# Kernel tuning notes

Measured on AMD Instinct MI355X. Metric: run time of the kernel, lower is better.

Reference implementation:

```python
import jax, jax.numpy as jnp
import numpy as np

B, L, D, H = 4, 1024, 1024, 16
HS = D // H
BLOCK = 1024
EPS = 1e-5


def setup_inputs() -> dict:
    key = jax.random.key(0)
    ks = jax.random.split(key, 12)
    s = 0.02
    return {
        "x": jax.random.normal(ks[0], (B, L, D), jnp.float32),
        "ln1_w": jnp.ones((D,), jnp.float32),
        "ln1_b": jnp.zeros((D,), jnp.float32),
        "Wqkv": jax.random.normal(ks[1], (D, 3 * D), jnp.float32) * s,
        "bqkv": jnp.zeros((3 * D,), jnp.float32),
        "Wproj": jax.random.normal(ks[2], (D, D), jnp.float32) * s,
        "bproj": jnp.zeros((D,), jnp.float32),
        "Er": jax.random.normal(ks[3], (BLOCK, HS), jnp.float32) * s,
        "ln2_w": jnp.ones((D,), jnp.float32),
        "ln2_b": jnp.zeros((D,), jnp.float32),
        "Wfc": jax.random.normal(ks[4], (D, 4 * D), jnp.float32) * s,
        "bfc": jnp.zeros((4 * D,), jnp.float32),
        "Wfc2": jax.random.normal(ks[5], (4 * D, D), jnp.float32) * s,
        "bfc2": jnp.zeros((D,), jnp.float32),
    }


def _layernorm(x, w, b):
    mu = jnp.mean(x, axis=-1, keepdims=True)
    var = jnp.mean(jnp.square(x - mu), axis=-1, keepdims=True)
    return (x - mu) * jax.lax.rsqrt(var + EPS) * w + b


def _skew(QEr):
    # Music-Transformer skew: pad one zero column on the left of last dim,
    # reshape (B,H,L,L+1) -> (B,H,L+1,L), drop first row.
    b, h, l, _ = QEr.shape
    padded = jnp.pad(QEr, ((0, 0), (0, 0), (0, 0), (1, 0)))
    return padded.reshape(b, h, l + 1, l)[:, :, 1:, :]


def _block(x, ln1_w, ln1_b, Wqkv, bqkv, Wproj, bproj, Er,
           ln2_w, ln2_b, Wfc, bfc, Wfc2, bfc2):
    b, l, d = x.shape
    # --- attention on ln_1(x) ---
    h = _layernorm(x, ln1_w, ln1_b)
    qkv = h @ Wqkv + bqkv                      # (B, L, 3D)
    q, k, v = jnp.split(qkv, 3, axis=-1)
    q = q.reshape(b, l, H, HS).transpose(0, 2, 1, 3)  # (B,H,L,hs)
    k = k.reshape(b, l, H, HS).transpose(0, 2, 1, 3)
    v = v.reshape(b, l, H, HS).transpose(0, 2, 1, 3)

    start = BLOCK - l
    Er_t = Er[start:, :].T                     # (hs, L)
    QEr = jnp.einsum('bhld,dm->bhlm', q, Er_t)  # (B,H,L,L)
    Srel = _skew(QEr)

    QKt = jnp.einsum('bhld,bhmd->bhlm', q, k)  # (B,H,L,L)
    scale = 1.0 / jnp.sqrt(jnp.asarray(HS, x.dtype))
    att = (QKt + Srel) * scale
    causal = jnp.tril(jnp.ones((l, l), bool))
    att = jnp.where(causal, att, jnp.asarray(-jnp.inf, att.dtype))
    att = jax.nn.softmax(att, axis=-1)
    y = jnp.einsum('bhlm,bhmd->bhld', att, v)  # (B,H,L,hs)
    y = y.transpose(0, 2, 1, 3).reshape(b, l, d)
    a = y @ Wproj + bproj

    x = x + a
    # --- MLP on ln_2(x) ---
    h2 = _layernorm(x, ln2_w, ln2_b)
    m = jax.nn.gelu(h2 @ Wfc + bfc, approximate=False) @ Wfc2 + bfc2
    return x + m


def reference(x, ln1_w, ln1_b, Wqkv, bqkv, Wproj, bproj, Er,
              ln2_w, ln2_b, Wfc, bfc, Wfc2, bfc2):
    return _block(x, ln1_w, ln1_b, Wqkv, bqkv, Wproj, bproj, Er,
                  ln2_w, ln2_b, Wfc, bfc, Wfc2, bfc2)
```

## Files before the change

### kernel.cpp

```cpp
#include <hip/hip_runtime.h>
#include <hip/hip_bf16.h>
#include <math.h>

typedef __attribute__((ext_vector_type(8))) __bf16 bf16x8;
typedef __attribute__((ext_vector_type(4))) float f32x4;

#define LL 1024
#define DD 1024
#define HH 16

#define GLOAD16(g, l)                                              \
  __builtin_amdgcn_global_load_lds(                                \
      (const __attribute__((address_space(1))) void*)(g),          \
      (__attribute__((address_space(3))) void*)(l), 16, 0, 0)

#define FENCE asm volatile("" ::: "memory")
#define BARRIER do { FENCE; __builtin_amdgcn_s_barrier(); FENCE; } while (0)
#define SCHEDB __builtin_amdgcn_sched_barrier(0)

__global__ __launch_bounds__(256) void transpose_cvt(const float* __restrict__ W,
                                                     __hip_bfloat16* __restrict__ Wt,
                                                     int R, int C) {
  __shared__ float tile[32][33];
  int tx = threadIdx.x;
  int r0 = blockIdx.y * 32, c0 = blockIdx.x * 32;
  int r = tx >> 3, c4 = (tx & 7) * 4;
  float4 v = *(const float4*)&W[(size_t)(r0 + r) * C + c0 + c4];
  tile[r][c4 + 0] = v.x; tile[r][c4 + 1] = v.y;
  tile[r][c4 + 2] = v.z; tile[r][c4 + 3] = v.w;
  __syncthreads();
  int c = tx >> 3, r4 = (tx & 7) * 4;
  __hip_bfloat16 o[4];
#pragma unroll
  for (int j = 0; j < 4; ++j) o[j] = __float2bfloat16(tile[r4 + j][c]);
  *(uint2*)&Wt[(size_t)(c0 + c) * R + r0 + r4] = *(const uint2*)o;
}

__global__ __launch_bounds__(256) void cvt_er(const float* __restrict__ Er,
                                              __hip_bfloat16* __restrict__ Erb) {
  int i = blockIdx.x * 256 + threadIdx.x;
  float4 v = *(const float4*)&Er[(size_t)i * 4];
  __hip_bfloat16 o[4];
  o[0] = __float2bfloat16(v.x); o[1] = __float2bfloat16(v.y);
  o[2] = __float2bfloat16(v.z); o[3] = __float2bfloat16(v.w);
  *(uint2*)&Erb[(size_t)i * 4] = *(const uint2*)o;
}

__global__ __launch_bounds__(256) void ln_kernel(const float* __restrict__ X,
                                                 const float* __restrict__ w,
                                                 const float* __restrict__ b,
                                                 __hip_bfloat16* __restrict__ out) {
  int row = blockIdx.x;
  int tid = threadIdx.x;
  const float* xr = X + (size_t)row * DD;
  float4 v = *(const float4*)&xr[tid * 4];
  float s = v.x + v.y + v.z + v.w;
  float s2 = v.x * v.x + v.y * v.y + v.z * v.z + v.w * v.w;
#pragma unroll
  for (int m = 1; m < 64; m <<= 1) {
    s += __shfl_xor(s, m);
    s2 += __shfl_xor(s2, m);
  }
  __shared__ float ps[4], ps2[4];
  int wv_ = tid >> 6, lane = tid & 63;
  if (lane == 0) { ps[wv_] = s; ps2[wv_] = s2; }
  __syncthreads();
  float ts = ps[0] + ps[1] + ps[2] + ps[3];
  float ts2 = ps2[0] + ps2[1] + ps2[2] + ps2[3];
  float mu = ts * (1.0f / DD);
  float var = ts2 * (1.0f / DD) - mu * mu;
  float rs = rsqrtf(var + 1e-5f);
  float4 wv = *(const float4*)&w[tid * 4];
  float4 bv = *(const float4*)&b[tid * 4];
  __hip_bfloat16 o[4];
  o[0] = __float2bfloat16((v.x - mu) * rs * wv.x + bv.x);
  o[1] = __float2bfloat16((v.y - mu) * rs * wv.y + bv.y);
  o[2] = __float2bfloat16((v.z - mu) * rs * wv.z + bv.z);
  o[3] = __float2bfloat16((v.w - mu) * rs * wv.w + bv.w);
  *(uint2*)&out[(size_t)row * DD + tid * 4] = *(const uint2*)o;
}

template <int EPI>
__global__ __launch_bounds__(512) void gemm256(const __hip_bfloat16* __restrict__ A,
                                               const __hip_bfloat16* __restrict__ Bt,
                                               const float* __restrict__ bias,
                                               const float* __restrict__ resid,
                                               void* __restrict__ Cout,
                                               int M, int N, int K) {
  __shared__ __hip_bfloat16 Ab[2][2][128][64];
  __shared__ __hip_bfloat16 Bb[2][2][128][64];
  const int tid = threadIdx.x, lane = tid & 63, w = tid >> 6;
  const int wm = w >> 2, wn = w & 3;

  int nbx = gridDim.x, nwg = nbx * gridDim.y;
  int orig = blockIdx.y * nbx + blockIdx.x;
  int cpx = nwg >> 3;
  int wgid = (orig & 7) * cpx + (orig >> 3);
  int bm0 = (wgid / nbx) * 256, bn0 = (wgid % nbx) * 256;

  const int srow = lane >> 3;
  const int scol = ((lane & 7) ^ srow) * 8;
  const int fr = lane & 15, kq = lane >> 4;

  auto stageA = [&](int d, int half, int k0) {
    const __hip_bfloat16* g0 =
        A + (size_t)(bm0 + half * 128 + w * 16 + srow) * K + k0 + scol;
    char* dst = (char*)&Ab[d][half][0][0] + w * 2048;
    GLOAD16(g0, dst);
    GLOAD16(g0 + (size_t)8 * K, dst + 1024);
  };
  auto stageB = [&](int d, int half, int k0) {
    const __hip_bfloat16* g0 =
        Bt + (size_t)(bn0 + half * 128 + w * 16 + srow) * K + k0 + scol;
    char* dst = (char*)&Bb[d][half][0][0] + w * 2048;
    GLOAD16(g0, dst);
    GLOAD16(g0 + (size_t)8 * K, dst + 1024);
  };
  auto ldA = [&](int d, int r, int ks) -> bf16x8 {
    int byte = r * 128 + (((ks * 32 + kq * 8) * 2) ^ ((r & 7) << 4));
    return *(const bf16x8*)((const char*)&Ab[d][wm][0][0] + byte);
  };
  auto ldB = [&](int d, int r, int ks) -> bf16x8 {
    int byte = r * 128 + (((ks * 32 + kq * 8) * 2) ^ ((r & 7) << 4));
    return *(const bf16x8*)((const char*)&Bb[d][wn >> 1][0][0] + byte);
  };

  f32x4 acc[8][4] = {};
  bf16x8 a0[8], a1[8], b0[4], b1[4];

  auto rdA = [&](bf16x8* dst, int d, int mfb) {
#pragma unroll
    for (int mf = 0; mf < 4; ++mf)
#pragma unroll
      for (int ks = 0; ks < 2; ++ks)
        dst[mf * 2 + ks] = ldA(d, (mfb + mf) * 16 + fr, ks);
  };
  auto rdB = [&](bf16x8* dst, int d, int nfb) {
#pragma unroll
    for (int nf = 0; nf < 2; ++nf)
#pragma unroll
      for (int ks = 0; ks < 2; ++ks)
        dst[nf * 2 + ks] = ldB(d, (wn & 1) * 64 + (nfb + nf) * 16 + fr, ks);
  };
  auto mmq = [&](int mo, int no, bf16x8* ar, bf16x8* br) {
    __builtin_amdgcn_s_setprio(1);
#pragma unroll
    for (int mf = 0; mf < 4; ++mf)
#pragma unroll
      for (int nf = 0; nf < 2; ++nf)
#pragma unroll
        for (int ks = 0; ks < 2; ++ks)
          acc[mo + mf][no + nf] = __builtin_amdgcn_mfma_f32_16x16x32_bf16(
              ar[mf * 2 + ks], br[nf * 2 + ks], acc[mo + mf][no + nf], 0, 0, 0);
    __builtin_amdgcn_s_setprio(0);
  };

  stageA(0, 0, 0); stageA(0, 1, 0);
  stageB(0, 0, 0); stageB(0, 1, 0);
  stageA(1, 0, 64); stageA(1, 1, 64);
  asm volatile("s_waitcnt vmcnt(4)" ::: "memory");
  BARRIER;

  const int niter = (K >> 6) >> 1;
  for (int i = 0; i < niter; ++i) {
    const bool last = (i == niter - 1);
    const int k1 = (2 * i + 1) * 64, k2 = (2 * i + 2) * 64, k3 = (2 * i + 3) * 64;
    rdA(a0, 0, 0); rdB(b0, 0, 0);
    stageB(1, 0, k1);
    BARRIER; SCHEDB; mmq(0, 0, a0, b0); SCHEDB; BARRIER;
    rdA(a1, 0, 4);
    stageB(1, 1, k1);
    BARRIER; SCHEDB; mmq(4, 0, a1, b0); SCHEDB; BARRIER;
    rdB(b1, 0, 2);
    if (!last) stageA(0, 0, k2);
    BARRIER; SCHEDB; mmq(0, 2, a0, b1); SCHEDB; BARRIER;
    if (!last) stageA(0, 1, k2);
    BARRIER; SCHEDB; mmq(4, 2, a1, b1); SCHEDB;
    if (last) { asm volatile("s_waitcnt vmcnt(0)" ::: "memory"); }
    else      { asm volatile("s_waitcnt vmcnt(4)" ::: "memory"); }
    BARRIER;
    rdA(a0, 1, 0); rdB(b0, 1, 0);
    if (!last) stageB(0, 0, k2);
    BARRIER; SCHEDB; mmq(0, 0, a0, b0); SCHEDB; BARRIER;
    rdA(a1, 1, 4);
    if (!last) stageB(0, 1, k2);
    BARRIER; SCHEDB; mmq(4, 0, a1, b0); SCHEDB; BARRIER;
    rdB(b1, 1, 2);
    if (!last) stageA(1, 0, k3);
    BARRIER; SCHEDB; mmq(0, 2, a0, b1); SCHEDB; BARRIER;
    if (!last) stageA(1, 1, k3);
    BARRIER; SCHEDB; mmq(4, 2, a1, b1); SCHEDB;
    if (last) { asm volatile("s_waitcnt vmcnt(0)" ::: "memory"); }
    else      { asm volatile("s_waitcnt vmcnt(4)" ::: "memory"); }
    BARRIER;
  }

#pragma unroll
  for (int nf = 0; nf < 4; ++nf) {
    int col = bn0 + wn * 64 + nf * 16 + fr;
    float bsv = bias[col];
#pragma unroll
    for (int mf = 0; mf < 8; ++mf) {
      int rowb = bm0 + wm * 128 + mf * 16 + (lane >> 4) * 4;
#pragma unroll
      for (int j = 0; j < 4; ++j) {
        int row = rowb + j;
        float v = acc[mf][nf][j] + bsv;
        if (EPI == 1) v = 0.5f * v * (1.0f + erff(v * 0.7071067811865476f));
        if (EPI == 2) {
          ((float*)Cout)[(size_t)row * N + col] = v + resid[(size_t)row * N + col];
        } else {
          ((__hip_bfloat16*)Cout)[(size_t)row * N + col] = __float2bfloat16(v);
        }
      }
    }
  }
}

template <int EPI>
__global__ __launch_bounds__(256) void gemm128p(const __hip_bfloat16* __restrict__ A,
                                                const __hip_bfloat16* __restrict__ Bt,
                                                const float* __restrict__ bias,
                                                const float* __restrict__ resid,
                                                void* __restrict__ Cout,
                                                int M, int N, int K) {
  __shared__ __hip_bfloat16 Ab[2][2][64][64];
  __shared__ __hip_bfloat16 Bb[2][2][64][64];
  const int tid = threadIdx.x, lane = tid & 63, w = tid >> 6;
  const int wm = w >> 1, wn = w & 1;

  int nbx = gridDim.x, nwg = nbx * gridDim.y;
  int orig = blockIdx.y * nbx + blockIdx.x;
  int cpx = nwg >> 3;
  int wgid = (orig & 7) * cpx + (orig >> 3);
  int bm0 = (wgid / nbx) * 128, bn0 = (wgid % nbx) * 128;

  const int srow = lane >> 3;
  const int scol = ((lane & 7) ^ srow) * 8;
  const int fr = lane & 15, kq = lane >> 4;

  auto stageA = [&](int d, int half, int k0) {
    const __hip_bfloat16* g0 =
        A + (size_t)(bm0 + half * 64 + w * 16 + srow) * K + k0 + scol;
    char* dst = (char*)&Ab[d][half][0][0] + w * 2048;
    GLOAD16(g0, dst);
    GLOAD16(g0 + (size_t)8 * K, dst + 1024);
  };
  auto stageB = [&](int d, int half, int k0) {
    const __hip_bfloat16* g0 =
        Bt + (size_t)(bn0 + half * 64 + w * 16 + srow) * K + k0 + scol;
    char* dst = (char*)&Bb[d][half][0][0] + w * 2048;
    GLOAD16(g0, dst);
    GLOAD16(g0 + (size_t)8 * K, dst + 1024);
  };
  auto ldA = [&](int d, int r, int ks) -> bf16x8 {
    int byte = r * 128 + (((ks * 32 + kq * 8) * 2) ^ ((r & 7) << 4));
    return *(const bf16x8*)((const char*)&Ab[d][wm][0][0] + byte);
  };
  auto ldB = [&](int d, int r, int ks) -> bf16x8 {
    int byte = r * 128 + (((ks * 32 + kq * 8) * 2) ^ ((r & 7) << 4));
    return *(const bf16x8*)((const char*)&Bb[d][wn][0][0] + byte);
  };

  f32x4 acc[4][4] = {};
  bf16x8 aA[8], b0[4], b1[4];

  auto rdA = [&](int d) {
#pragma unroll
    for (int mf = 0; mf < 4; ++mf)
#pragma unroll
      for (int ks = 0; ks < 2; ++ks)
        aA[mf * 2 + ks] = ldA(d, mf * 16 + fr, ks);
  };
  auto rdB = [&](bf16x8* dst, int d, int nfb) {
#pragma unroll
    for (int nf = 0; nf < 2; ++nf)
#pragma unroll
      for (int ks = 0; ks < 2; ++ks)
        dst[nf * 2 + ks] = ldB(d, (nfb + nf) * 16 + fr, ks);
  };
  auto mmq = [&](int no, bf16x8* br) {
    __builtin_amdgcn_s_setprio(1);
#pragma unroll
    for (int mf = 0; mf < 4; ++mf)
#pragma unroll
      for (int nf = 0; nf < 2; ++nf)
#pragma unroll
        for (int ks = 0; ks < 2; ++ks)
          acc[mf][no + nf] = __builtin_amdgcn_mfma_f32_16x16x32_bf16(
              aA[mf * 2 + ks], br[nf * 2 + ks], acc[mf][no + nf], 0, 0, 0);
    __builtin_amdgcn_s_setprio(0);
  };

  stageA(0, 0, 0); stageA(0, 1, 0);
  stageB(0, 0, 0); stageB(0, 1, 0);
  stageA(1, 0, 64); stageA(1, 1, 64);
  asm volatile("s_waitcnt vmcnt(4)" ::: "memory");
  BARRIER;

  const int niter = (K >> 6) >> 1;
  for (int i = 0; i < niter; ++i) {
    const bool last = (i == niter - 1);
    const int k1 = (2 * i + 1) * 64, k2 = (2 * i + 2) * 64, k3 = (2 * i + 3) * 64;
    rdA(0); rdB(b0, 0, 0);
    stageB(1, 0, k1); stageB(1, 1, k1);
    BARRIER; SCHEDB; mmq(0, b0); SCHEDB; BARRIER;
    rdB(b1, 0, 2);
    if (!last) { stageA(0, 0, k2); stageA(0, 1, k2); }
    BARRIER; SCHEDB; mmq(2, b1); SCHEDB;
    if (last) { asm volatile("s_waitcnt vmcnt(0)" ::: "memory"); }
    else      { asm volatile("s_waitcnt vmcnt(4)" ::: "memory"); }
    BARRIER;
    rdA(1); rdB(b0, 1, 0);
    if (!last) { stageB(0, 0, k2); stageB(0, 1, k2); }
    BARRIER; SCHEDB; mmq(0, b0); SCHEDB; BARRIER;
    rdB(b1, 1, 2);
    if (!last) { stageA(1, 0, k3); stageA(1, 1, k3); }
    BARRIER; SCHEDB; mmq(2, b1); SCHEDB;
    if (last) { asm volatile("s_waitcnt vmcnt(0)" ::: "memory"); }
    else      { asm volatile("s_waitcnt vmcnt(4)" ::: "memory"); }
    BARRIER;
  }

#pragma unroll
  for (int nf = 0; nf < 4; ++nf) {
    int col = bn0 + wn * 64 + nf * 16 + fr;
    float bsv = bias[col];
#pragma unroll
    for (int mf = 0; mf < 4; ++mf) {
      int rowb = bm0 + wm * 64 + mf * 16 + (lane >> 4) * 4;
#pragma unroll
      for (int j = 0; j < 4; ++j) {
        int row = rowb + j;
        float v = acc[mf][nf][j] + bsv;
        if (EPI == 1) v = 0.5f * v * (1.0f + erff(v * 0.7071067811865476f));
        if (EPI == 2) {
          ((float*)Cout)[(size_t)row * N + col] = v + resid[(size_t)row * N + col];
        } else {
          ((__hip_bfloat16*)Cout)[(size_t)row * N + col] = __float2bfloat16(v);
        }
      }
    }
  }
}

__global__ __launch_bounds__(256) void attn_mfma(const __hip_bfloat16* __restrict__ qkv,
                                                 const __hip_bfloat16* __restrict__ Erb,
                                                 __hip_bfloat16* __restrict__ Y) {
  __shared__ __hip_bfloat16 k_s[64][72];
  __shared__ __hip_bfloat16 er_s[128][72];
  __shared__ __hip_bfloat16 p_s[4][16][72];
  __shared__ __hip_bfloat16 g_s[4][16][128];
  __shared__ __hip_bfloat16 vt_s[64 * 64];

  int bid = blockIdx.x;
  int qi = 15 - (bid >> 6);
  int head = bid & 63;
  int h = head & 15, b = head >> 4;
  int l0 = qi * 64;
  int tid = threadIdx.x, lane = tid & 63, w = tid >> 6;
  const int fr = lane & 15, kq = lane >> 4;

  const __hip_bfloat16* base = qkv + (size_t)b * (LL * 3072) + h * 64;

  bf16x8 qf[2];
  {
    const __hip_bfloat16* q0 = base + (size_t)(l0 + 16 * w + fr) * 3072 + kq * 8;
    qf[0] = *(const bf16x8*)q0;
    qf[1] = *(const bf16x8*)(q0 + 32);
  }

  const int ksr = tid >> 2, ksd = (tid & 3) * 16;
  const __hip_bfloat16* ksrc = base + 1024 + (size_t)ksr * 3072 + ksd;
  const int vc = (tid >> 3) * 2, vd0 = (tid & 7) * 8;
  const __hip_bfloat16* vsrc = base + 2048 + (size_t)vc * 3072 + vd0;
  const int e0r = tid >> 1, e0c = (tid & 1) * 32;
  const int err = tid >> 2, erc = (tid & 3) * 16;

  uint4 kst0, kst1, vst0, vst1;
  uint4 est0, est1, est2, est3;
  uint4 ers0, ers1;

  {
    kst0 = *(const uint4*)ksrc; kst1 = *(const uint4*)(ksrc + 8);
    vst0 = *(const uint4*)vsrc; vst1 = *(const uint4*)(vsrc + 3072);
    int m = min(max(960 - l0 + e0r, 0), 1023);
    const __hip_bfloat16* ep = Erb + (size_t)m * 64 + e0c;
    est0 = *(const uint4*)ep;        est1 = *(const uint4*)(ep + 8);
    est2 = *(const uint4*)(ep + 16); est3 = *(const uint4*)(ep + 24);
  }

  f32x4 oacc[4] = {};
  float m_run[4], s_run[4];
#pragma unroll
  for (int j = 0; j < 4; ++j) { m_run[j] = -1e30f; s_run[j] = 0.f; }

  auto gchunk = [&](int hf) {
#pragma unroll
    for (int g = 0; g < 4; ++g) {
      int cc = hf * 64 + 16 * g + fr, kc = kq * 8;
      bf16x8 e0 = *(const bf16x8*)&er_s[cc][kc];
      bf16x8 e1 = *(const bf16x8*)&er_s[cc][kc + 32];
      f32x4 gacc = {};
      gacc = __builtin_amdgcn_mfma_f32_16x16x32_bf16(qf[0], e0, gacc, 0, 0, 0);
      gacc = __builtin_amdgcn_mfma_f32_16x16x32_bf16(qf[1], e1, gacc, 0, 0, 0);
#pragma unroll
      for (int j = 0; j < 4; ++j)
        g_s[w][kq * 4 + j][hf * 64 + 16 * g + fr] = __float2bfloat16(gacc[j]);
    }
  };

  for (int t = 0; t <= qi; ++t) {
    __syncthreads();
    *(uint4*)&k_s[ksr][ksd] = kst0;
    *(uint4*)&k_s[ksr][ksd + 8] = kst1;
    {
      const uint16_t* h0 = (const uint16_t*)&vst0;
      const uint16_t* h1 = (const uint16_t*)&vst1;
#pragma unroll
      for (int j = 0; j < 8; ++j) {
        int d = vd0 + j;
        uint32_t pk = (uint32_t)h0[j] | ((uint32_t)h1[j] << 16);
        uint32_t byte = ((uint32_t)d << 7) + 2u * (uint32_t)vc;
        byte ^= (uint32_t)(((d & 7) ^ (d >> 3)) << 4);
        *(uint32_t*)((char*)vt_s + byte) = pk;
      }
    }
    if (t == 0) {
      *(uint4*)&er_s[e0r][e0c]      = est0;
      *(uint4*)&er_s[e0r][e0c + 8]  = est1;
      *(uint4*)&er_s[e0r][e0c + 16] = est2;
      *(uint4*)&er_s[e0r][e0c + 24] = est3;
    } else if (t < qi) {
      int hf = (t + 1) & 1;
      *(uint4*)&er_s[hf * 64 + err][erc]     = ers0;
      *(uint4*)&er_s[hf * 64 + err][erc + 8] = ers1;
    }
    __syncthreads();
    if (t < qi) {
      int c0n = (t + 1) * 64;
      const __hip_bfloat16* kp = ksrc + (size_t)c0n * 3072;
      kst0 = *(const uint4*)kp; kst1 = *(const uint4*)(kp + 8);
      const __hip_bfloat16* vp = vsrc + (size_t)c0n * 3072;
      vst0 = *(const uint4*)vp; vst1 = *(const uint4*)(vp + 3072);
      if (t + 1 < qi) {
        int m = min(960 - l0 + (t + 2) * 64 + err, 1023);
        const __hip_bfloat16* ep = Erb + (size_t)m * 64 + erc;
        ers0 = *(const uint4*)ep; ers1 = *(const uint4*)(ep + 8);
      }
    }
    SCHEDB;

    f32x4 sacc[4] = {};
#pragma unroll
    for (int f = 0; f < 4; ++f) {
      int cc = 16 * f + fr, kc = kq * 8;
      bf16x8 k0 = *(const bf16x8*)&k_s[cc][kc];
      bf16x8 k1 = *(const bf16x8*)&k_s[cc][kc + 32];
      sacc[f] = __builtin_amdgcn_mfma_f32_16x16x32_bf16(qf[0], k0, sacc[f], 0, 0, 0);
      sacc[f] = __builtin_amdgcn_mfma_f32_16x16x32_bf16(qf[1], k1, sacc[f], 0, 0, 0);
    }
    if (t == 0) {
      gchunk(0);
      if (qi > 0) gchunk(1);
    } else if (t < qi) {
      gchunk((t + 1) & 1);
    }

    float sv[4][4];
#pragma unroll
    for (int f = 0; f < 4; ++f) {
#pragma unroll
      for (int j = 0; j < 4; ++j) {
        int r = kq * 4 + j;
        int c = 16 * f + fr;
        int jj = c - (16 * w + r) + 63;
        float g = __bfloat162float(g_s[w][r][(t * 64 + jj) & 127]);
        float val = (sacc[f][j] + g) * 0.125f;
        if (t == qi && c > 16 * w + r) val = -1e30f;
        sv[f][j] = val;
      }
    }
    float alpha[4];
#pragma unroll
    for (int j = 0; j < 4; ++j) {
      float tm = fmaxf(fmaxf(sv[0][j], sv[1][j]), fmaxf(sv[2][j], sv[3][j]));
      tm = fmaxf(tm, __shfl_xor(tm, 1));
      tm = fmaxf(tm, __shfl_xor(tm, 2));
      tm = fmaxf(tm, __shfl_xor(tm, 4));
      tm = fmaxf(tm, __shfl_xor(tm, 8));
      float nm = fmaxf(m_run[j], tm);
      alpha[j] = __expf(m_run[j] - nm);
      m_run[j] = nm;
    }
#pragma unroll
    for (int f = 0; f < 4; ++f)
#pragma unroll
      for (int j = 0; j < 4; ++j)
        sv[f][j] = __expf(sv[f][j] - m_run[j]);
#pragma unroll
    for (int j = 0; j < 4; ++j) {
      float ps = sv[0][j] + sv[1][j] + sv[2][j] + sv[3][j];
      ps += __shfl_xor(ps, 1); ps += __shfl_xor(ps, 2);
      ps += __shfl_xor(ps, 4); ps += __shfl_xor(ps, 8);
      s_run[j] = s_run[j] * alpha[j] + ps;
    }
#pragma unroll
    for (int f = 0; f < 4; ++f)
#pragma unroll
      for (int j = 0; j < 4; ++j)
        oacc[f][j] *= alpha[j];
#pragma unroll
    for (int f = 0; f < 4; ++f)
#pragma unroll
      for (int j = 0; j < 4; ++j)
        p_s[w][kq * 4 + j][16 * f + fr] = __float2bfloat16(sv[f][j]);
#pragma unroll
    for (int kk = 0; kk < 2; ++kk) {
      bf16x8 pf = *(const bf16x8*)&p_s[w][fr][kq * 8 + 32 * kk];
#pragma unroll
      for (int f = 0; f < 4; ++f) {
        int d = 16 * f + fr;
        int cc = kq * 8 + 32 * kk;
        uint32_t byte = ((uint32_t)d << 7) + 2u * (uint32_t)cc;
        byte ^= (uint32_t)(((d & 7) ^ (d >> 3)) << 4);
        bf16x8 vf = *(const bf16x8*)((char*)vt_s + byte);
        oacc[f] = __builtin_amdgcn_mfma_f32_16x16x32_bf16(pf, vf, oacc[f], 0, 0, 0);
      }
    }
  }

#pragma unroll
  for (int f = 0; f < 4; ++f)
#pragma unroll
    for (int j = 0; j < 4; ++j) {
      int r = 16 * w + kq * 4 + j;
      int d = 16 * f + fr;
      float o = oacc[f][j] / s_run[j];
      Y[(size_t)(b * LL + l0 + r) * DD + h * 64 + d] = __float2bfloat16(o);
    }
}

extern "C" void kernel_launch(void* const* d_in, const int* in_sizes, int n_in,
                              void* d_out, int out_size, void* d_ws, size_t ws_size,
                              hipStream_t stream) {
  (void)in_sizes; (void)n_in; (void)out_size; (void)ws_size;
  const float* x     = (const float*)d_in[0];
  const float* ln1w  = (const float*)d_in[1];
  const float* ln1b  = (const float*)d_in[2];
  const float* Wqkv  = (const float*)d_in[3];
  const float* bqkv  = (const float*)d_in[4];
  const float* Wproj = (const float*)d_in[5];
  const float* bproj = (const float*)d_in[6];
  const float* Er    = (const float*)d_in[7];
  const float* ln2w  = (const float*)d_in[8];
  const float* ln2b  = (const float*)d_in[9];
  const float* Wfc   = (const float*)d_in[10];
  const float* bfc   = (const float*)d_in[11];
  const float* Wfc2  = (const float*)d_in[12];
  const float* bfc2  = (const float*)d_in[13];
  float* out = (float*)d_out;

  char* ws = (char*)d_ws;
  const size_t MB = 1ull << 20;
  __hip_bfloat16* h1    = (__hip_bfloat16*)(ws + 0);
  __hip_bfloat16* qkvb  = (__hip_bfloat16*)(ws + 8 * MB);
  __hip_bfloat16* mbuf  = (__hip_bfloat16*)(ws + 0);
  __hip_bfloat16* yb    = (__hip_bfloat16*)(ws + 32 * MB);
  __hip_bfloat16* h2    = (__hip_bfloat16*)(ws + 32 * MB);
  float*          x2    = (float*)(ws + 40 * MB);
  __hip_bfloat16* Wqkvt = (__hip_bfloat16*)(ws + 56 * MB);
  __hip_bfloat16* Erb   = (__hip_bfloat16*)(ws + 62 * MB);
  __hip_bfloat16* Wprojt= (__hip_bfloat16*)(ws + 63 * MB);
  __hip_bfloat16* Wfct  = (__hip_bfloat16*)(ws + 66 * MB);
  __hip_bfloat16* Wfc2t = (__hip_bfloat16*)(ws + 75 * MB);

  dim3 blk(256);

  transpose_cvt<<<dim3(3072 / 32, 1024 / 32), blk, 0, stream>>>(Wqkv, Wqkvt, 1024, 3072);
  transpose_cvt<<<dim3(1024 / 32, 1024 / 32), blk, 0, stream>>>(Wproj, Wprojt, 1024, 1024);
  transpose_cvt<<<dim3(4096 / 32, 1024 / 32), blk, 0, stream>>>(Wfc, Wfct, 1024, 4096);
  transpose_cvt<<<dim3(1024 / 32, 4096 / 32), blk, 0, stream>>>(Wfc2, Wfc2t, 4096, 1024);
  cvt_er<<<dim3(64), blk, 0, stream>>>(Er, Erb);

  ln_kernel<<<4096, blk, 0, stream>>>(x, ln1w, ln1b, h1);

  gemm256<0><<<dim3(3072 / 256, 4096 / 256), dim3(512), 0, stream>>>(
      h1, Wqkvt, bqkv, nullptr, qkvb, 4096, 3072, 1024);

  attn_mfma<<<dim3(1024), blk, 0, stream>>>(qkvb, Erb, yb);

  gemm128p<2><<<dim3(1024 / 128, 4096 / 128), blk, 0, stream>>>(
      yb, Wprojt, bproj, x, x2, 4096, 1024, 1024);

  ln_kernel<<<4096, blk, 0, stream>>>(x2, ln2w, ln2b, h2);

  gemm256<1><<<dim3(4096 / 256, 4096 / 256), dim3(512), 0, stream>>>(
      h2, Wfct, bfc, nullptr, mbuf, 4096, 4096, 1024);

  gemm128p<2><<<dim3(1024 / 128, 4096 / 128), blk, 0, stream>>>(
      mbuf, Wfc2t, bfc2, x2, out, 4096, 1024, 4096);
}
```

Measured before the change: 261.9 us.

## Restructure GEMM pipelines to deeper multi-stage K=32 ring buffers

Both GEMM kernels drop the double-buffered K=64 staging in favour of a ring of K=32 LDS stages: four stages for the 256 tile and five for the 128 tile. Loads are issued three or four tiles ahead, with matching vmcnt waits and a new XOR swizzle for 64-byte rows. The intent is to keep more global loads in flight and hide memory latency, at the cost of more barriers per unit of K and smaller MFMA batches per sync.

```diff
diff --git a/kernel.cpp b/kernel.cpp
--- a/kernel.cpp
+++ b/kernel.cpp
@@ -87,8 +87,8 @@
                                                const float* __restrict__ resid,
                                                void* __restrict__ Cout,
                                                int M, int N, int K) {
-  __shared__ __hip_bfloat16 Ab[2][2][128][64];
-  __shared__ __hip_bfloat16 Bb[2][2][128][64];
+  __shared__ __hip_bfloat16 Ab[4][256][32];
+  __shared__ __hip_bfloat16 Bb[4][256][32];
   const int tid = threadIdx.x, lane = tid & 63, w = tid >> 6;
   const int wm = w >> 2, wn = w & 3;
 
@@ -98,100 +98,67 @@
   int wgid = (orig & 7) * cpx + (orig >> 3);
   int bm0 = (wgid / nbx) * 256, bn0 = (wgid % nbx) * 256;
 
-  const int srow = lane >> 3;
-  const int scol = ((lane & 7) ^ srow) * 8;
   const int fr = lane & 15, kq = lane >> 4;
-
-  auto stageA = [&](int d, int half, int k0) {
-    const __hip_bfloat16* g0 =
-        A + (size_t)(bm0 + half * 128 + w * 16 + srow) * K + k0 + scol;
-    char* dst = (char*)&Ab[d][half][0][0] + w * 2048;
-    GLOAD16(g0, dst);
-    GLOAD16(g0 + (size_t)8 * K, dst + 1024);
-  };
-  auto stageB = [&](int d, int half, int k0) {
-    const __hip_bfloat16* g0 =
-        Bt + (size_t)(bn0 + half * 128 + w * 16 + srow) * K + k0 + scol;
-    char* dst = (char*)&Bb[d][half][0][0] + w * 2048;
-    GLOAD16(g0, dst);
-    GLOAD16(g0 + (size_t)8 * K, dst + 1024);
-  };
-  auto ldA = [&](int d, int r, int ks) -> bf16x8 {
-    int byte = r * 128 + (((ks * 32 + kq * 8) * 2) ^ ((r & 7) << 4));
-    return *(const bf16x8*)((const char*)&Ab[d][wm][0][0] + byte);
-  };
-  auto ldB = [&](int d, int r, int ks) -> bf16x8 {
-    int byte = r * 128 + (((ks * 32 + kq * 8) * 2) ^ ((r & 7) << 4));
-    return *(const bf16x8*)((const char*)&Bb[d][wn >> 1][0][0] + byte);
+  const int sg = ((lane & 3) ^ ((lane >> 3) & 3)) * 8;
+  const int srw = lane >> 2;
+
+  auto stageA = [&](int c, int half, int k0) {
+    const __hip_bfloat16* src =
+        A + (size_t)(bm0 + half * 128 + w * 16 + srw) * K + k0 + sg;
+    GLOAD16(src, (char*)Ab + c * 16384 + half * 8192 + w * 1024);
+  };
+  auto stageB = [&](int c, int half, int k0) {
+    const __hip_bfloat16* src =
+        Bt + (size_t)(bn0 + half * 128 + w * 16 + srw) * K + k0 + sg;
+    GLOAD16(src, (char*)Bb + c * 16384 + half * 8192 + w * 1024);
+  };
+  const int swz = ((kq ^ ((fr >> 1) & 3)) << 4);
+  auto ldA = [&](int c, int r) -> bf16x8 {
+    return *(const bf16x8*)((const char*)Ab + c * 16384 + r * 64 + swz);
+  };
+  auto ldB = [&](int c, int r) -> bf16x8 {
+    return *(const bf16x8*)((const char*)Bb + c * 16384 + r * 64 + swz);
   };
 
   f32x4 acc[8][4] = {};
-  bf16x8 a0[8], a1[8], b0[4], b1[4];
-
-  auto rdA = [&](bf16x8* dst, int d, int mfb) {
-#pragma unroll
-    for (int mf = 0; mf < 4; ++mf)
-#pragma unroll
-      for (int ks = 0; ks < 2; ++ks)
-        dst[mf * 2 + ks] = ldA(d, (mfb + mf) * 16 + fr, ks);
-  };
-  auto rdB = [&](bf16x8* dst, int d, int nfb) {
-#pragma unroll
-    for (int nf = 0; nf < 2; ++nf)
-#pragma unroll
-      for (int ks = 0; ks < 2; ++ks)
-        dst[nf * 2 + ks] = ldB(d, (wn & 1) * 64 + (nfb + nf) * 16 + fr, ks);
-  };
-  auto mmq = [&](int mo, int no, bf16x8* ar, bf16x8* br) {
+  bf16x8 a[8], b0[2], b1[2];
+
+  auto mm16 = [&](int no, bf16x8* br) {
     __builtin_amdgcn_s_setprio(1);
 #pragma unroll
-    for (int mf = 0; mf < 4; ++mf)
+    for (int mf = 0; mf < 8; ++mf)
 #pragma unroll
       for (int nf = 0; nf < 2; ++nf)
-#pragma unroll
-        for (int ks = 0; ks < 2; ++ks)
-          acc[mo + mf][no + nf] = __builtin_amdgcn_mfma_f32_16x16x32_bf16(
-              ar[mf * 2 + ks], br[nf * 2 + ks], acc[mo + mf][no + nf], 0, 0, 0);
+        acc[mf][no + nf] = __builtin_amdgcn_mfma_f32_16x16x32_bf16(
+            a[mf], br[nf], acc[mf][no + nf], 0, 0, 0);
     __builtin_amdgcn_s_setprio(0);
   };
 
-  stageA(0, 0, 0); stageA(0, 1, 0);
-  stageB(0, 0, 0); stageB(0, 1, 0);
-  stageA(1, 0, 64); stageA(1, 1, 64);
-  asm volatile("s_waitcnt vmcnt(4)" ::: "memory");
+  const int nt = K >> 5;
+#pragma unroll
+  for (int tt = 0; tt < 3; ++tt) {
+    stageA(tt, 0, tt * 32); stageA(tt, 1, tt * 32);
+    stageB(tt, 0, tt * 32); stageB(tt, 1, tt * 32);
+  }
+  asm volatile("s_waitcnt vmcnt(8)" ::: "memory");
   BARRIER;
 
-  const int niter = (K >> 6) >> 1;
-  for (int i = 0; i < niter; ++i) {
-    const bool last = (i == niter - 1);
-    const int k1 = (2 * i + 1) * 64, k2 = (2 * i + 2) * 64, k3 = (2 * i + 3) * 64;
-    rdA(a0, 0, 0); rdB(b0, 0, 0);
-    stageB(1, 0, k1);
-    BARRIER; SCHEDB; mmq(0, 0, a0, b0); SCHEDB; BARRIER;
-    rdA(a1, 0, 4);
-    stageB(1, 1, k1);
-    BARRIER; SCHEDB; mmq(4, 0, a1, b0); SCHEDB; BARRIER;
-    rdB(b1, 0, 2);
-    if (!last) stageA(0, 0, k2);
-    BARRIER; SCHEDB; mmq(0, 2, a0, b1); SCHEDB; BARRIER;
-    if (!last) stageA(0, 1, k2);
-    BARRIER; SCHEDB; mmq(4, 2, a1, b1); SCHEDB;
-    if (last) { asm volatile("s_waitcnt vmcnt(0)" ::: "memory"); }
-    else      { asm volatile("s_waitcnt vmcnt(4)" ::: "memory"); }
-    BARRIER;
-    rdA(a0, 1, 0); rdB(b0, 1, 0);
-    if (!last) stageB(0, 0, k2);
-    BARRIER; SCHEDB; mmq(0, 0, a0, b0); SCHEDB; BARRIER;
-    rdA(a1, 1, 4);
-    if (!last) stageB(0, 1, k2);
-    BARRIER; SCHEDB; mmq(4, 0, a1, b0); SCHEDB; BARRIER;
-    rdB(b1, 1, 2);
-    if (!last) stageA(1, 0, k3);
-    BARRIER; SCHEDB; mmq(0, 2, a0, b1); SCHEDB; BARRIER;
-    if (!last) stageA(1, 1, k3);
-    BARRIER; SCHEDB; mmq(4, 2, a1, b1); SCHEDB;
-    if (last) { asm volatile("s_waitcnt vmcnt(0)" ::: "memory"); }
-    else      { asm volatile("s_waitcnt vmcnt(4)" ::: "memory"); }
+  for (int t = 0; t < nt; ++t) {
+    const int cur = t & 3, nxt = (t + 3) & 3, kn = (t + 3) * 32;
+    const bool st = (t + 3 < nt);
+#pragma unroll
+    for (int mf = 0; mf < 8; ++mf) a[mf] = ldA(cur, wm * 128 + mf * 16 + fr);
+#pragma unroll
+    for (int nf = 0; nf < 2; ++nf) b0[nf] = ldB(cur, wn * 64 + nf * 16 + fr);
+    if (st) { stageA(nxt, 0, kn); stageA(nxt, 1, kn); }
+    BARRIER; SCHEDB; mm16(0, b0); SCHEDB; BARRIER;
+#pragma unroll
+    for (int nf = 0; nf < 2; ++nf) b1[nf] = ldB(cur, wn * 64 + (nf + 2) * 16 + fr);
+    if (st) { stageB(nxt, 0, kn); stageB(nxt, 1, kn); }
+    BARRIER; SCHEDB; mm16(2, b1); SCHEDB;
+    if (t <= nt - 4)      { asm volatile("s_waitcnt vmcnt(8)" ::: "memory"); }
+    else if (t == nt - 3) { asm volatile("s_waitcnt vmcnt(4)" ::: "memory"); }
+    else if (t == nt - 2) { asm volatile("s_waitcnt vmcnt(0)" ::: "memory"); }
     BARRIER;
   }
 
@@ -201,7 +168,7 @@
     float bsv = bias[col];
 #pragma unroll
     for (int mf = 0; mf < 8; ++mf) {
-      int rowb = bm0 + wm * 128 + mf * 16 + (lane >> 4) * 4;
+      int rowb = bm0 + wm * 128 + mf * 16 + kq * 4;
 #pragma unroll
       for (int j = 0; j < 4; ++j) {
         int row = rowb + j;
@@ -224,8 +191,8 @@
                                                 const float* __restrict__ resid,
                                                 void* __restrict__ Cout,
                                                 int M, int N, int K) {
-  __shared__ __hip_bfloat16 Ab[2][2][64][64];
-  __shared__ __hip_bfloat16 Bb[2][2][64][64];
+  __shared__ __hip_bfloat16 Ab[5][128][32];
+  __shared__ __hip_bfloat16 Bb[5][128][32];
   const int tid = threadIdx.x, lane = tid & 63, w = tid >> 6;
   const int wm = w >> 1, wn = w & 1;
 
@@ -235,91 +202,68 @@
   int wgid = (orig & 7) * cpx + (orig >> 3);
   int bm0 = (wgid / nbx) * 128, bn0 = (wgid % nbx) * 128;
 
-  const int srow = lane >> 3;
-  const int scol = ((lane & 7) ^ srow) * 8;
   const int fr = lane & 15, kq = lane >> 4;
-
-  auto stageA = [&](int d, int half, int k0) {
-    const __hip_bfloat16* g0 =
-        A + (size_t)(bm0 + half * 64 + w * 16 + srow) * K + k0 + scol;
-    char* dst = (char*)&Ab[d][half][0][0] + w * 2048;
-    GLOAD16(g0, dst);
-    GLOAD16(g0 + (size_t)8 * K, dst + 1024);
-  };
-  auto stageB = [&](int d, int half, int k0) {
-    const __hip_bfloat16* g0 =
-        Bt + (size_t)(bn0 + half * 64 + w * 16 + srow) * K + k0 + scol;
-    char* dst = (char*)&Bb[d][half][0][0] + w * 2048;
-    GLOAD16(g0, dst);
-    GLOAD16(g0 + (size_t)8 * K, dst + 1024);
-  };
-  auto ldA = [&](int d, int r, int ks) -> bf16x8 {
-    int byte = r * 128 + (((ks * 32 + kq * 8) * 2) ^ ((r & 7) << 4));
-    return *(const bf16x8*)((const char*)&Ab[d][wm][0][0] + byte);
-  };
-  auto ldB = [&](int d, int r, int ks) -> bf16x8 {
-    int byte = r * 128 + (((ks * 32 + kq * 8) * 2) ^ ((r & 7) << 4));
-    return *(const bf16x8*)((const char*)&Bb[d][wn][0][0] + byte);
+  const int sg = ((lane & 3) ^ ((lane >> 3) & 3)) * 8;
+  const int srw = lane >> 2;
+
+  auto stageA = [&](int c, int half, int k0) {
+    const __hip_bfloat16* src =
+        A + (size_t)(bm0 + half * 64 + w * 16 + srw) * K + k0 + sg;
+    GLOAD16(src, (char*)Ab + c * 8192 + half * 4096 + w * 1024);
+  };
+  auto stageB = [&](int c, int half, int k0) {
+    const __hip_bfloat16* src =
+        Bt + (size_t)(bn0 + half * 64 + w * 16 + srw) * K + k0 + sg;
+    GLOAD16(src, (char*)Bb + c * 8192 + half * 4096 + w * 1024);
+  };
+  const int swz = ((kq ^ ((fr >> 1) & 3)) << 4);
+  auto ldA = [&](int c, int r) -> bf16x8 {
+    return *(const bf16x8*)((const char*)Ab + c * 8192 + r * 64 + swz);
+  };
+  auto ldB = [&](int c, int r) -> bf16x8 {
+    return *(const bf16x8*)((const char*)Bb + c * 8192 + r * 64 + swz);
   };
 
   f32x4 acc[4][4] = {};
-  bf16x8 aA[8], b0[4], b1[4];
-
-  auto rdA = [&](int d) {
+  bf16x8 a[4], b[4];
+
+  const int nt = K >> 5;
+#pragma unroll
+  for (int tt = 0; tt < 4; ++tt) {
+    stageA(tt, 0, tt * 32); stageA(tt, 1, tt * 32);
+    stageB(tt, 0, tt * 32); stageB(tt, 1, tt * 32);
+  }
+  asm volatile("s_waitcnt vmcnt(12)" ::: "memory");
+  BARRIER;
+
+  int cur = 0, nxt = 4;
+  for (int t = 0; t < nt; ++t) {
+    const int kn = (t + 4) * 32;
+    const bool st = (t + 4 < nt);
+#pragma unroll
+    for (int mf = 0; mf < 4; ++mf) a[mf] = ldA(cur, wm * 64 + mf * 16 + fr);
+#pragma unroll
+    for (int nf = 0; nf < 4; ++nf) b[nf] = ldB(cur, wn * 64 + nf * 16 + fr);
+    if (st) {
+      stageA(nxt, 0, kn); stageA(nxt, 1, kn);
+      stageB(nxt, 0, kn); stageB(nxt, 1, kn);
+    }
+    BARRIER; SCHEDB;
+    __builtin_amdgcn_s_setprio(1);
 #pragma unroll
     for (int mf = 0; mf < 4; ++mf)
 #pragma unroll
-      for (int ks = 0; ks < 2; ++ks)
-        aA[mf * 2 + ks] = ldA(d, mf * 16 + fr, ks);
-  };
-  auto rdB = [&](bf16x8* dst, int d, int nfb) {
-#pragma unroll
-    for (int nf = 0; nf < 2; ++nf)
-#pragma unroll
-      for (int ks = 0; ks < 2; ++ks)
-        dst[nf * 2 + ks] = ldB(d, (nfb + nf) * 16 + fr, ks);
-  };
-  auto mmq = [&](int no, bf16x8* br) {
-    __builtin_amdgcn_s_setprio(1);
-#pragma unroll
-    for (int mf = 0; mf < 4; ++mf)
-#pragma unroll
-      for (int nf = 0; nf < 2; ++nf)
-#pragma unroll
-        for (int ks = 0; ks < 2; ++ks)
-          acc[mf][no + nf] = __builtin_amdgcn_mfma_f32_16x16x32_bf16(
-              aA[mf * 2 + ks], br[nf * 2 + ks], acc[mf][no + nf], 0, 0, 0);
+      for (int nf = 0; nf < 4; ++nf)
+        acc[mf][nf] = __builtin_amdgcn_mfma_f32_16x16x32_bf16(a[mf], b[nf], acc[mf][nf], 0, 0, 0);
     __builtin_amdgcn_s_setprio(0);
-  };
-
-  stageA(0, 0, 0); stageA(0, 1, 0);
-  stageB(0, 0, 0); stageB(0, 1, 0);
-  stageA(1, 0, 64); stageA(1, 1, 64);
-  asm volatile("s_waitcnt vmcnt(4)" ::: "memory");
-  BARRIER;
-
-  const int niter = (K >> 6) >> 1;
-  for (int i = 0; i < niter; ++i) {
-    const bool last = (i == niter - 1);
-    const int k1 = (2 * i + 1) * 64, k2 = (2 * i + 2) * 64, k3 = (2 * i + 3) * 64;
-    rdA(0); rdB(b0, 0, 0);
-    stageB(1, 0, k1); stageB(1, 1, k1);
-    BARRIER; SCHEDB; mmq(0, b0); SCHEDB; BARRIER;
-    rdB(b1, 0, 2);
-    if (!last) { stageA(0, 0, k2); stageA(0, 1, k2); }
-    BARRIER; SCHEDB; mmq(2, b1); SCHEDB;
-    if (last) { asm volatile("s_waitcnt vmcnt(0)" ::: "memory"); }
-    else      { asm volatile("s_waitcnt vmcnt(4)" ::: "memory"); }
+    SCHEDB;
+    if (t <= nt - 5)      { asm volatile("s_waitcnt vmcnt(12)" ::: "memory"); }
+    else if (t == nt - 4) { asm volatile("s_waitcnt vmcnt(8)" ::: "memory"); }
+    else if (t == nt - 3) { asm volatile("s_waitcnt vmcnt(4)" ::: "memory"); }
+    else if (t == nt - 2) { asm volatile("s_waitcnt vmcnt(0)" ::: "memory"); }
     BARRIER;
-    rdA(1); rdB(b0, 1, 0);
-    if (!last) { stageB(0, 0, k2); stageB(0, 1, k2); }
-    BARRIER; SCHEDB; mmq(0, b0); SCHEDB; BARRIER;
-    rdB(b1, 1, 2);
-    if (!last) { stageA(1, 0, k3); stageA(1, 1, k3); }
-    BARRIER; SCHEDB; mmq(2, b1); SCHEDB;
-    if (last) { asm volatile("s_waitcnt vmcnt(0)" ::: "memory"); }
-    else      { asm volatile("s_waitcnt vmcnt(4)" ::: "memory"); }
-    BARRIER;
+    cur = (cur == 4) ? 0 : cur + 1;
+    nxt = (nxt == 4) ? 0 : nxt + 1;
   }
 
 #pragma unroll
@@ -328,7 +272,7 @@
     float bsv = bias[col];
 #pragma unroll
     for (int mf = 0; mf < 4; ++mf) {
-      int rowb = bm0 + wm * 64 + mf * 16 + (lane >> 4) * 4;
+      int rowb = bm0 + wm * 64 + mf * 16 + kq * 4;
 #pragma unroll
       for (int j = 0; j < 4; ++j) {
         int row = rowb + j;
```

After: 255.5 us. 1.02x faster.
